# Performance work log

Hardware: AMD Instinct MI355X
Metric: run time of the kernel (lower is better)

Reference implementation:

```python
import jax, jax.numpy as jnp
import numpy as np

B, S, D = 64, 1452, 1024
G, K, R = 288, 4, 32
VIS = 1152  # number of vision patch tokens; tail is S - VIS = 300 text tokens
MAX_TOKENS = 300


def setup_inputs() -> dict:
    key = jax.random.key(0)
    k1, k2, k3, k4 = jax.random.split(key, 4)
    hidden_states = jax.random.normal(k1, (B, S, D), dtype=jnp.float32)
    attention_mask = jnp.ones((B, S), dtype=jnp.int32)
    # all batches share the same vision patch range [0, VIS-1]
    patch_range_list = jnp.tile(jnp.array([[0, VIS - 1]], dtype=jnp.int32), (B, 1))
    base = jnp.broadcast_to(jnp.arange(VIS, dtype=jnp.int32).reshape(1, G, K), (B, G, K))
    drop = jax.random.uniform(k2, (B, G, K)) < 0.1
    patch_indices_list_list = jnp.where(drop, jnp.int32(-1), base)
    rem = jax.random.randint(k3, (B, R), 0, VIS, dtype=jnp.int32)
    rem = jnp.where(jax.random.uniform(k4, (B, R)) < 0.25, jnp.int32(-1), rem)
    return {
        "hidden_states": hidden_states,
        "attention_mask": attention_mask,
        "patch_range_list": patch_range_list,
        "patch_indices_list_list": patch_indices_list_list,
        "remove_index_list_list": rem,
    }


def reference(hidden_states, attention_mask, patch_range_list, patch_indices_list_list, remove_index_list_list):
    Bn, Sn, Dn = hidden_states.shape
    _, Gn, Kn = patch_indices_list_list.shape
    # vision_end_token_index is taken from batch 0 in the original and used for a
    # shape-defining slice; treat as static (identical across batches here).
    vis_end = int(patch_range_list[0, 1]) + 1

    start = patch_range_list[:, 0]            # [B]
    end = patch_range_list[:, 1]              # [B]
    L = end - start + 1                       # [B] length of sliced hidden_state

    idx = patch_indices_list_list             # [B,G,K]
    mask = idx != -1                          # [B,G,K]
    # remove_index_list: drop -1 padding (map to -2 sentinel so it never matches)
    rem = jnp.where(remove_index_list_list == -1, jnp.int32(-2), remove_index_list_list)  # [B,R]
    in_rem = (idx[..., None] == rem[:, None, None, :]).any(-1)  # torch.isin, [B,G,K]
    mask = mask & ~in_rem

    # torch gather with -1 wraps to the last element of the SLICED hidden_state;
    # replicate exactly (note: the original sums wrapped/removed entries too).
    idx_w = jnp.where(idx >= 0, idx, idx + L[:, None, None])
    gidx = start[:, None, None] + idx_w       # absolute indices into hidden_states
    gathered = jnp.take_along_axis(
        hidden_states, gidx.reshape(Bn, Gn * Kn, 1), axis=1
    ).reshape(Bn, Gn, Kn, Dn)

    cnt = mask.sum(-1)                        # [B,G] divisor = count of kept entries
    pooled = gathered.sum(2) / jnp.maximum(cnt, 1)[..., None].astype(hidden_states.dtype)

    # rows with no valid entries are dropped; survivors are written right-aligned
    valid = mask.any(-1)                      # [B,G]
    n_valid = valid.sum(1)                    # [B]
    rank = jnp.cumsum(valid, axis=1) - 1      # 0-based rank among valid rows
    pos = jnp.where(valid, MAX_TOKENS - n_valid[:, None] + rank, MAX_TOKENS)  # OOB -> drop
    bidx = jnp.arange(Bn)[:, None]

    out_head = jnp.zeros((Bn, MAX_TOKENS, Dn), hidden_states.dtype).at[bidx, pos].set(pooled, mode="drop")
    att_head = jnp.zeros((Bn, MAX_TOKENS), attention_mask.dtype).at[bidx, pos].set(1, mode="drop")

    outputs = jnp.concatenate([out_head, hidden_states[:, vis_end:]], axis=1)
    outputs_attention = jnp.concatenate([att_head, attention_mask[:, vis_end:]], axis=1)
    return outputs, outputs_attention
```

## Files before the change

kernel.cpp:

```cpp
#include <hip/hip_runtime.h>
#include <hip/hip_bf16.h>

#define Bn 64
#define Sn 1452
#define Dn 1024
#define Gn 288
#define Kn 4
#define Rn 32
#define MAXT 300

typedef float f32x4 __attribute__((ext_vector_type(4)));

__global__ void __launch_bounds__(512)
phaseA_kernel(const int* __restrict__ idx,
              const int* __restrict__ rem,
              const int* __restrict__ attn,
              int* __restrict__ cnt_ws,
              int* __restrict__ gor_ws,
              int* __restrict__ nv_ws,
              float* __restrict__ att_out,
              int vis_end, int T) {
    const int b = blockIdx.x;
    const int tid = threadIdx.x;

    __shared__ int s_rem[Rn];
    __shared__ int s_wsum[8];

    if (tid < Rn) {
        int r = rem[b * Rn + tid];
        s_rem[tid] = (r == -1) ? -2 : r;
    }
    __syncthreads();

    int cnt = 0;
    if (tid < Gn) {
#pragma unroll
        for (int k = 0; k < Kn; ++k) {
            int v = idx[(b * Gn + tid) * Kn + k];
            bool m = (v != -1);
            if (m) {
#pragma unroll
                for (int r = 0; r < Rn; ++r) {
                    if (v == s_rem[r]) { m = false; }
                }
            }
            cnt += m ? 1 : 0;
        }
        cnt_ws[b * Gn + tid] = cnt;
    }

    const int valid = (tid < Gn && cnt > 0) ? 1 : 0;
    const unsigned long long m = __ballot(valid);
    const int lane = tid & 63;
    const int w = tid >> 6;
    if (lane == 0) s_wsum[w] = __popcll(m);
    __syncthreads();

    int off = 0, tot = 0;
#pragma unroll
    for (int i = 0; i < 8; ++i) {
        int v = s_wsum[i];
        tot += v;
        if (i < w) off += v;
    }
    if (valid) {
        int rank = off + __popcll(m & ((1ull << lane) - 1ull));
        gor_ws[b * Gn + rank] = tid;
    }
    if (tid == 0) nv_ws[b] = tot;

    const int nvalid = tot;
    for (int t = tid; t < T; t += 512) {
        float v;
        if (t < MAXT) {
            v = (t >= MAXT - nvalid) ? 1.0f : 0.0f;
        } else {
            v = (float)attn[b * Sn + vis_end + (t - MAXT)];
        }
        att_out[(size_t)b * T + t] = v;
    }
}

__global__ void __launch_bounds__(256)
head_kernel(const float* __restrict__ hs,
            const int* __restrict__ idx,
            const int* __restrict__ pr,
            const int* __restrict__ cnt_ws,
            const int* __restrict__ gor_ws,
            const int* __restrict__ nv_ws,
            float* __restrict__ out,
            int T) {
    const int t = blockIdx.x;
    const int b = blockIdx.y;
    const int tid = threadIdx.x;

    f32x4* outp = (f32x4*)(out + ((size_t)b * T + t) * Dn);

    const int nvalid = nv_ws[b];
    if (t < MAXT - nvalid) {
        f32x4 z = {0.f, 0.f, 0.f, 0.f};
        __builtin_nontemporal_store(z, &outp[tid]);
        return;
    }

    const int g = gor_ws[b * Gn + (t - (MAXT - nvalid))];
    const int start = pr[b * 2];
    const int L = pr[b * 2 + 1] - start + 1;

    f32x4 acc = {0.f, 0.f, 0.f, 0.f};
#pragma unroll
    for (int k = 0; k < Kn; ++k) {
        int v = idx[(b * Gn + g) * Kn + k];
        int w = (v >= 0) ? v : v + L;
        const f32x4* row = (const f32x4*)(hs + ((size_t)b * Sn + start + w) * Dn);
        acc += row[tid];
    }
    const int c = cnt_ws[b * Gn + g];
    const float scale = 1.0f / (float)((c > 1) ? c : 1);
    acc *= scale;
    __builtin_nontemporal_store(acc, &outp[tid]);
}

__global__ void __launch_bounds__(256)
tail_kernel(const float* __restrict__ hs,
            float* __restrict__ out,
            int vis_end, int T, int tail4) {
    const int c = blockIdx.x;
    const int b = blockIdx.y;
    const int tid = threadIdx.x;

    const f32x4* src = (const f32x4*)(hs + ((size_t)b * Sn + vis_end) * Dn);
    f32x4* dst = (f32x4*)(out + ((size_t)b * T + MAXT) * Dn);

    const int base = c * 1024;
    f32x4 v0, v1, v2, v3;
    int e0 = base + 0 * 256 + tid;
    int e1 = base + 1 * 256 + tid;
    int e2 = base + 2 * 256 + tid;
    int e3 = base + 3 * 256 + tid;
    bool p0 = e0 < tail4, p1 = e1 < tail4, p2 = e2 < tail4, p3 = e3 < tail4;
    if (p0) v0 = __builtin_nontemporal_load(&src[e0]);
    if (p1) v1 = __builtin_nontemporal_load(&src[e1]);
    if (p2) v2 = __builtin_nontemporal_load(&src[e2]);
    if (p3) v3 = __builtin_nontemporal_load(&src[e3]);
    if (p0) __builtin_nontemporal_store(v0, &dst[e0]);
    if (p1) __builtin_nontemporal_store(v1, &dst[e1]);
    if (p2) __builtin_nontemporal_store(v2, &dst[e2]);
    if (p3) __builtin_nontemporal_store(v3, &dst[e3]);
}

extern "C" void kernel_launch(void* const* d_in, const int* in_sizes, int n_in,
                              void* d_out, int out_size, void* d_ws, size_t ws_size,
                              hipStream_t stream) {
    const float* hs  = (const float*)d_in[0];
    const int* attn  = (const int*)d_in[1];
    const int* pr    = (const int*)d_in[2];
    const int* idx   = (const int*)d_in[3];
    const int* rem   = (const int*)d_in[4];

    float* out = (float*)d_out;

    const int T = out_size / (Bn * (Dn + 1));
    const int vis_end = Sn - (T - MAXT);

    float* att_out = out + (size_t)Bn * T * Dn;

    int* cnt_ws = (int*)d_ws;
    int* gor_ws = cnt_ws + Bn * Gn;
    int* nv_ws  = gor_ws + Bn * Gn;

    const int tail_rows = T - MAXT;
    const int tail4 = tail_rows * (Dn / 4);
    const int nchunks = (tail_rows + 3) / 4;

    phaseA_kernel<<<Bn, 512, 0, stream>>>(idx, rem, attn, cnt_ws, gor_ws, nv_ws,
                                          att_out, vis_end, T);
    tail_kernel<<<dim3(nchunks, Bn), 256, 0, stream>>>(hs, out, vis_end, T, tail4);
    head_kernel<<<dim3(MAXT, Bn), 256, 0, stream>>>(hs, idx, pr, cnt_ws, gor_ws, nv_ws,
                                                    out, T);
}
```

Before: 89.01 us.

## Merge tail copy and head pooling into one launch with two rows per block

Fuses the tail copy kernel and the head pooling kernel into a single rows_kernel whose grid covers both head blocks and tail chunks, removing one kernel launch and the gap between the two. Each head block now handles two output rows, halving the head block count and giving each block more loads in flight. The cost is a branch-divergent block role and possible imbalance between short head blocks and tail-copy blocks.

```diff
diff --git a/kernel.cpp b/kernel.cpp
--- a/kernel.cpp
+++ b/kernel.cpp
@@ -82,71 +82,70 @@
 }
 
 __global__ void __launch_bounds__(256)
-head_kernel(const float* __restrict__ hs,
+rows_kernel(const float* __restrict__ hs,
             const int* __restrict__ idx,
             const int* __restrict__ pr,
             const int* __restrict__ cnt_ws,
             const int* __restrict__ gor_ws,
             const int* __restrict__ nv_ws,
             float* __restrict__ out,
-            int T) {
-    const int t = blockIdx.x;
+            int vis_end, int T, int nheadblk, int tail4) {
+    const int x = blockIdx.x;
     const int b = blockIdx.y;
     const int tid = threadIdx.x;
 
-    f32x4* outp = (f32x4*)(out + ((size_t)b * T + t) * Dn);
+    if (x >= nheadblk) {
+        const int c = x - nheadblk;
+        const f32x4* src = (const f32x4*)(hs + ((size_t)b * Sn + vis_end) * Dn);
+        f32x4* dst = (f32x4*)(out + ((size_t)b * T + MAXT) * Dn);
 
-    const int nvalid = nv_ws[b];
-    if (t < MAXT - nvalid) {
-        f32x4 z = {0.f, 0.f, 0.f, 0.f};
-        __builtin_nontemporal_store(z, &outp[tid]);
+        const int base = c * 1024;
+        f32x4 v0, v1, v2, v3;
+        int e0 = base + 0 * 256 + tid;
+        int e1 = base + 1 * 256 + tid;
+        int e2 = base + 2 * 256 + tid;
+        int e3 = base + 3 * 256 + tid;
+        bool p0 = e0 < tail4, p1 = e1 < tail4, p2 = e2 < tail4, p3 = e3 < tail4;
+        if (p0) v0 = __builtin_nontemporal_load(&src[e0]);
+        if (p1) v1 = __builtin_nontemporal_load(&src[e1]);
+        if (p2) v2 = __builtin_nontemporal_load(&src[e2]);
+        if (p3) v3 = __builtin_nontemporal_load(&src[e3]);
+        if (p0) __builtin_nontemporal_store(v0, &dst[e0]);
+        if (p1) __builtin_nontemporal_store(v1, &dst[e1]);
+        if (p2) __builtin_nontemporal_store(v2, &dst[e2]);
+        if (p3) __builtin_nontemporal_store(v3, &dst[e3]);
         return;
     }
 
-    const int g = gor_ws[b * Gn + (t - (MAXT - nvalid))];
+    const int nvalid = nv_ws[b];
+    const int zcut = MAXT - nvalid;
     const int start = pr[b * 2];
     const int L = pr[b * 2 + 1] - start + 1;
 
-    f32x4 acc = {0.f, 0.f, 0.f, 0.f};
 #pragma unroll
-    for (int k = 0; k < Kn; ++k) {
-        int v = idx[(b * Gn + g) * Kn + k];
-        int w = (v >= 0) ? v : v + L;
-        const f32x4* row = (const f32x4*)(hs + ((size_t)b * Sn + start + w) * Dn);
-        acc += row[tid];
+    for (int i = 0; i < 2; ++i) {
+        const int t = 2 * x + i;
+        if (t >= MAXT) break;
+        f32x4* outp = (f32x4*)(out + ((size_t)b * T + t) * Dn);
+        if (t < zcut) {
+            f32x4 z = {0.f, 0.f, 0.f, 0.f};
+            __builtin_nontemporal_store(z, &outp[tid]);
+            continue;
+        }
+        const int g = gor_ws[b * Gn + (t - zcut)];
+        f32x4 acc = {0.f, 0.f, 0.f, 0.f};
+#pragma unroll
+        for (int k = 0; k < Kn; ++k) {
+            int v = idx[(b * Gn + g) * Kn + k];
+            int w = (v >= 0) ? v : v + L;
+            const f32x4* row = (const f32x4*)(hs + ((size_t)b * Sn + start + w) * Dn);
+            acc += row[tid];
+        }
+        const int c = cnt_ws[b * Gn + g];
+        const float scale = 1.0f / (float)((c > 1) ? c : 1);
+        acc *= scale;
+        __builtin_nontemporal_store(acc, &outp[tid]);
     }
-    const int c = cnt_ws[b * Gn + g];
-    const float scale = 1.0f / (float)((c > 1) ? c : 1);
-    acc *= scale;
-    __builtin_nontemporal_store(acc, &outp[tid]);
-}
-
-__global__ void __launch_bounds__(256)
-tail_kernel(const float* __restrict__ hs,
-            float* __restrict__ out,
-            int vis_end, int T, int tail4) {
-    const int c = blockIdx.x;
-    const int b = blockIdx.y;
-    const int tid = threadIdx.x;
-
-    const f32x4* src = (const f32x4*)(hs + ((size_t)b * Sn + vis_end) * Dn);
-    f32x4* dst = (f32x4*)(out + ((size_t)b * T + MAXT) * Dn);
-
-    const int base = c * 1024;
-    f32x4 v0, v1, v2, v3;
-    int e0 = base + 0 * 256 + tid;
-    int e1 = base + 1 * 256 + tid;
-    int e2 = base + 2 * 256 + tid;
-    int e3 = base + 3 * 256 + tid;
-    bool p0 = e0 < tail4, p1 = e1 < tail4, p2 = e2 < tail4, p3 = e3 < tail4;
-    if (p0) v0 = __builtin_nontemporal_load(&src[e0]);
-    if (p1) v1 = __builtin_nontemporal_load(&src[e1]);
-    if (p2) v2 = __builtin_nontemporal_load(&src[e2]);
-    if (p3) v3 = __builtin_nontemporal_load(&src[e3]);
-    if (p0) __builtin_nontemporal_store(v0, &dst[e0]);
-    if (p1) __builtin_nontemporal_store(v1, &dst[e1]);
-    if (p2) __builtin_nontemporal_store(v2, &dst[e2]);
-    if (p3) __builtin_nontemporal_store(v3, &dst[e3]);
 }
 
 extern "C" void kernel_launch(void* const* d_in, const int* in_sizes, int n_in,
@@ -171,11 +170,11 @@
 
     const int tail_rows = T - MAXT;
     const int tail4 = tail_rows * (Dn / 4);
-    const int nchunks = (tail_rows + 3) / 4;
+    const int ntail = (tail_rows + 3) / 4;
+    const int nheadblk = (MAXT + 1) / 2;
 
     phaseA_kernel<<<Bn, 512, 0, stream>>>(idx, rem, attn, cnt_ws, gor_ws, nv_ws,
                                           att_out, vis_end, T);
-    tail_kernel<<<dim3(nchunks, Bn), 256, 0, stream>>>(hs, out, vis_end, T, tail4);
-    head_kernel<<<dim3(MAXT, Bn), 256, 0, stream>>>(hs, idx, pr, cnt_ws, gor_ws, nv_ws,
-                                                    out, T);
+    rows_kernel<<<dim3(nheadblk + ntail, Bn), 256, 0, stream>>>(
+        hs, idx, pr, cnt_ws, gor_ws, nv_ws, out, vis_end, T, nheadblk, tail4);
 }
```

New measurement: 83.05 us. 6.7% less time.
